# Kernel optimization log

Hardware: AMD Instinct MI355X
Metric: run time of the kernel (lower is better)

The kernel has to match this reference:

```python
import jax, jax.numpy as jnp
import numpy as np
import math

OVERLAP_RATIO = 0.5
TAU_OVERLAP = 0.07
TAU_TILE = 0.2
TILE_LOSS_WEIGHT = 0.1


def setup_inputs() -> dict:
    key = jax.random.key(0)
    k1, k2 = jax.random.split(key)
    B, V, S, D = 8, 8, 576, 768
    z1 = jax.random.normal(k1, (B * V, S, D), dtype=jnp.float32)
    z2 = jax.random.normal(k2, (B * V, S, D), dtype=jnp.float32)
    # module expects L2-normalised projections
    z1 = z1 / jnp.linalg.norm(z1, axis=-1, keepdims=True)
    z2 = z2 / jnp.linalg.norm(z2, axis=-1, keepdims=True)
    return {"z1": z1, "z2": z2, "batch_size": B, "num_views": V}


def _sym_infonce_diag(logits):
    # logits: [..., N, N]; labels are the diagonal (same index positives).
    lse_q = jax.nn.logsumexp(logits, axis=-1)  # row-wise (q -> k)
    lse_k = jax.nn.logsumexp(logits, axis=-2)  # col-wise (k -> q), no transpose copy
    diag = jnp.diagonal(logits, axis1=-2, axis2=-1)
    return 0.5 * (jnp.mean(lse_q - diag) + jnp.mean(lse_k - diag))


def reference(z1, z2, batch_size, num_views):
    B, V = batch_size, num_views
    z1 = z1.astype(jnp.float32)
    z2 = z2.astype(jnp.float32)
    BV, S, D = z1.shape
    H = W = int(math.isqrt(S))

    # ---- overlap InfoNCE (circular adjacency) ----
    g1 = z1.reshape(B, V, H, W, D)
    g2 = z2.reshape(B, V, H, W, D)
    k = max(1, int(W * OVERLAP_RATIO))
    N = B * H * k
    curr_right = g1[:, :, :, -k:, :]                      # [B,V,H,k,D]
    next_left = jnp.roll(g2, -1, axis=1)[:, :, :, :k, :]  # [B,V,H,k,D]
    Q = jnp.transpose(curr_right, (1, 0, 2, 3, 4)).reshape(V, N, D)
    K = jnp.transpose(next_left, (1, 0, 2, 3, 4)).reshape(V, N, D)
    ov_logits = jnp.einsum('vnd,vmd->vnm', Q, K) / TAU_OVERLAP  # [V,N,N]
    L_overlap = _sym_infonce_diag(ov_logits)

    # ---- within-tile InfoNCE ----
    tile_logits = jnp.einsum('bsd,btd->bst', z1, z2) / TAU_TILE  # [BV,S,S]
    L_tile = _sym_infonce_diag(tile_logits)

    total = L_overlap + TILE_LOSS_WEIGHT * L_tile
    return total
```

## Files before the change

### kernel.cpp

```cpp
#include <hip/hip_runtime.h>
#include <hip/hip_bf16.h>

typedef __attribute__((ext_vector_type(8))) short bf16x8_t;
typedef __attribute__((ext_vector_type(4))) float f32x4_t;
typedef __attribute__((ext_vector_type(8))) unsigned short u16x8_t;

__device__ inline unsigned short bfr(float f) {
    __hip_bfloat16 h = __float2bfloat16(f);
    return *reinterpret_cast<unsigned short*>(&h);
}

__device__ inline u16x8_t cvt8(float4 x, float4 y) {
    u16x8_t v;
    v[0] = bfr(x.x); v[1] = bfr(x.y); v[2] = bfr(x.z); v[3] = bfr(x.w);
    v[4] = bfr(y.x); v[5] = bfr(y.y); v[6] = bfr(y.z); v[7] = bfr(y.w);
    return v;
}

__global__ __launch_bounds__(256, 4) void gemm128_lse_all(
    const float* __restrict__ z1, const float* __restrict__ z2,
    float* __restrict__ ws) {
    const int tid  = threadIdx.x;
    const int lane = tid & 63;
    const int w    = tid >> 6;
    const int wM   = w >> 1;
    const int wN   = w & 1;
    const int lr   = lane & 15;
    const int lg   = lane >> 4;

    const int bid = blockIdx.x;
    const int lb  = (bid & 7) * 524 + (bid >> 3);

    int M, batch, brow, bcol;
    float inv_tau;
    float *rs, *cs, *dg;
    bool ov = (lb < 2592);
    if (ov) {
        M = 2304; inv_tau = 1.0f / 0.07f;
        rs = ws; cs = ws + 18432; dg = ws + 36864;
        batch = lb / 324;
        int rem = lb - batch * 324;
        int sc = rem / 108, r2 = rem - sc * 108;
        brow = r2 / 6;
        bcol = sc * 6 + (r2 - brow * 6);
    } else {
        M = 576; inv_tau = 1.0f / 0.2f;
        rs = ws + 55296; cs = ws + 92160; dg = ws + 129024;
        int tl = lb - 2592;
        batch = tl / 25;
        int rem = tl - batch * 25;
        brow = rem / 5;
        bcol = rem - brow * 5;
    }

    __shared__ unsigned short smem[16384];
    __shared__ int offA[128], offB[128];

    if (tid < 128) {
        int r = brow * 128 + tid;
        int off;
        if (ov) {
            int b = r / 288, rm = r % 288, h = rm / 12, j = rm % 12;
            off = ((b * 8 + batch) * 576 + h * 24 + 12 + j) * 768;
        } else {
            off = ((r < M) ? (batch * 576 + r) : (batch * 576)) * 768;
        }
        offA[tid] = off;
    } else {
        int c = bcol * 128 + (tid - 128);
        int off;
        if (ov) {
            int b = c / 288, rm = c % 288, h = rm / 12, j = rm % 12;
            off = ((b * 8 + ((batch + 1) & 7)) * 576 + h * 24 + j) * 768;
        } else {
            off = ((c < M) ? (batch * 576 + c) : (batch * 576)) * 768;
        }
        offB[tid - 128] = off;
    }
    __syncthreads();

    const int lrow8 = lane >> 3;
    const int cswz  = (((lane & 7) ^ lrow8) << 3);
    int sA[4], sB[4], dA[4], dB[4];
#pragma unroll
    for (int ra = 0; ra < 4; ++ra) {
        sA[ra] = offA[w * 32 + ra * 8 + lrow8] + cswz;
        sB[ra] = offB[w * 32 + ra * 8 + lrow8] + cswz;
        dA[ra] = (w * 32 + ra * 8) * 64 + lane * 8;
        dB[ra] = 8192 + (w * 32 + ra * 8) * 64 + lane * 8;
    }

    int aoff[2][4], boff[2][4];
#pragma unroll
    for (int h = 0; h < 2; ++h) {
#pragma unroll
        for (int i = 0; i < 4; ++i) {
            int ra = wM * 64 + i * 16 + lr;
            aoff[h][i] = ra * 64 + (((h * 4 + lg) ^ (ra & 7)) << 3);
            int rb = wN * 64 + i * 16 + lr;
            boff[h][i] = 8192 + rb * 64 + (((h * 4 + lg) ^ (rb & 7)) << 3);
        }
    }

    f32x4_t acc[4][4];
#pragma unroll
    for (int i = 0; i < 4; ++i)
#pragma unroll
        for (int j = 0; j < 4; ++j) acc[i][j] = (f32x4_t){0.f, 0.f, 0.f, 0.f};

    for (int t = 0; t < 12; ++t) {
        const int k0 = t * 64;
        {
            float4 fa[8];
#pragma unroll
            for (int ra = 0; ra < 4; ++ra) {
                fa[2 * ra]     = *(const float4*)(z1 + sA[ra] + k0);
                fa[2 * ra + 1] = *(const float4*)(z1 + sA[ra] + k0 + 4);
            }
#pragma unroll
            for (int ra = 0; ra < 4; ++ra)
                *(u16x8_t*)&smem[dA[ra]] = cvt8(fa[2 * ra], fa[2 * ra + 1]);
        }
        {
            float4 fb[8];
#pragma unroll
            for (int ra = 0; ra < 4; ++ra) {
                fb[2 * ra]     = *(const float4*)(z2 + sB[ra] + k0);
                fb[2 * ra + 1] = *(const float4*)(z2 + sB[ra] + k0 + 4);
            }
#pragma unroll
            for (int ra = 0; ra < 4; ++ra)
                *(u16x8_t*)&smem[dB[ra]] = cvt8(fb[2 * ra], fb[2 * ra + 1]);
        }
        __syncthreads();
#pragma unroll
        for (int h = 0; h < 2; ++h) {
            bf16x8_t av[4], bv[4];
#pragma unroll
            for (int i = 0; i < 4; ++i) av[i] = *(const bf16x8_t*)&smem[aoff[h][i]];
#pragma unroll
            for (int j = 0; j < 4; ++j) bv[j] = *(const bf16x8_t*)&smem[boff[h][j]];
            __builtin_amdgcn_s_setprio(1);
#pragma unroll
            for (int i = 0; i < 4; ++i)
#pragma unroll
                for (int j = 0; j < 4; ++j)
                    acc[i][j] = __builtin_amdgcn_mfma_f32_16x16x32_bf16(
                        av[i], bv[j], acc[i][j], 0, 0, 0);
            __builtin_amdgcn_s_setprio(0);
        }
        __syncthreads();
    }

    const int rowbase = brow * 128 + wM * 64;
    const int colbase = bcol * 128 + wN * 64;
    float colacc[4] = {0.f, 0.f, 0.f, 0.f};
#pragma unroll
    for (int i = 0; i < 4; ++i) {
#pragma unroll
        for (int reg = 0; reg < 4; ++reg) {
            int row = rowbase + i * 16 + lg * 4 + reg;
            bool rv = row < M;
            float rp = 0.f;
#pragma unroll
            for (int j = 0; j < 4; ++j) {
                int col = colbase + j * 16 + lr;
                float L = acc[i][j][reg] * inv_tau;
                float e = (rv && (col < M)) ? __expf(L) : 0.f;
                rp += e;
                colacc[j] += e;
                if (rv && row == col) dg[batch * M + row] = L;
            }
#pragma unroll
            for (int s = 1; s < 16; s <<= 1) rp += __shfl_xor(rp, s);
            if (lr == 0 && rv) atomicAdd(&rs[batch * M + row], rp);
        }
    }
#pragma unroll
    for (int j = 0; j < 4; ++j) {
        float cv = colacc[j];
        cv += __shfl_xor(cv, 16);
        cv += __shfl_xor(cv, 32);
        int col = colbase + j * 16 + lr;
        if (lg == 0 && col < M) atomicAdd(&cs[batch * M + col], cv);
    }
}

__global__ __launch_bounds__(256) void finalize_kernel(
    const float* __restrict__ ws, float* __restrict__ out) {
    const float* rs_ov = ws;
    const float* cs_ov = ws + 18432;
    const float* dg_ov = ws + 36864;
    const float* rs_t  = ws + 55296;
    const float* cs_t  = ws + 92160;
    const float* dg_t  = ws + 129024;
    const int g0 = blockIdx.x * blockDim.x + threadIdx.x;
    const int gs = gridDim.x * blockDim.x;
    float s_ov = 0.f, s_t = 0.f;
    for (int i = g0; i < 18432; i += gs)
        s_ov += logf(rs_ov[i]) + logf(cs_ov[i]) - 2.f * dg_ov[i];
    for (int i = g0; i < 36864; i += gs)
        s_t += logf(rs_t[i]) + logf(cs_t[i]) - 2.f * dg_t[i];
    float c = 0.5f * s_ov / 18432.f + 0.05f * s_t / 36864.f;
#pragma unroll
    for (int s = 1; s < 64; s <<= 1) c += __shfl_xor(c, s);
    __shared__ float red[4];
    int wv = threadIdx.x >> 6;
    if ((threadIdx.x & 63) == 0) red[wv] = c;
    __syncthreads();
    if (threadIdx.x == 0)
        atomicAdd(out, red[0] + red[1] + red[2] + red[3]);
}

extern "C" void kernel_launch(void* const* d_in, const int* in_sizes, int n_in,
                              void* d_out, int out_size, void* d_ws, size_t ws_size,
                              hipStream_t stream) {
    const float* z1 = (const float*)d_in[0];
    const float* z2 = (const float*)d_in[1];
    float* out = (float*)d_out;
    float* ws  = (float*)d_ws;

    const size_t ACC_B = 165888 * sizeof(float);
    hipMemsetAsync(d_ws, 0, ACC_B, stream);
    hipMemsetAsync(d_out, 0, sizeof(float), stream);

    gemm128_lse_all<<<4192, 256, 0, stream>>>(z1, z2, ws);
    finalize_kernel<<<16, 256, 0, stream>>>(ws, out);
}
```

Baseline: 189.1 us.

## Enlarge GEMM tile to 256x256 with 1024-thread blocks and double-buffered LDS

Each block now computes a 256x256 output tile with 16 waves instead of 128x128 with 4 waves, so each global fp32 element is loaded and converted to bf16 about half as often. The K loop uses 32-wide slices with two LDS buffers, staging the next slice before computing the current one, which removes one barrier per step. The cost is a much lower block count (1224 vs 4192), one block per CU, more padding waste on the 576-wide tile GEMMs (3x3 tiles of 256 cover 768), and more barrier steps over the shorter K slices.

```diff
diff --git a/kernel.cpp b/kernel.cpp
--- a/kernel.cpp
+++ b/kernel.cpp
@@ -17,47 +17,47 @@
     return v;
 }
 
-__global__ __launch_bounds__(256, 4) void gemm128_lse_all(
+__global__ __launch_bounds__(1024, 1) void gemm256_lse_all(
     const float* __restrict__ z1, const float* __restrict__ z2,
     float* __restrict__ ws) {
     const int tid  = threadIdx.x;
     const int lane = tid & 63;
     const int w    = tid >> 6;
-    const int wM   = w >> 1;
-    const int wN   = w & 1;
+    const int wr   = w >> 2;
+    const int wc   = w & 3;
     const int lr   = lane & 15;
     const int lg   = lane >> 4;
 
     const int bid = blockIdx.x;
-    const int lb  = (bid & 7) * 524 + (bid >> 3);
+    const int lb  = (bid & 7) * 153 + (bid >> 3);
 
     int M, batch, brow, bcol;
     float inv_tau;
     float *rs, *cs, *dg;
-    bool ov = (lb < 2592);
+    bool ov = (lb < 648);
     if (ov) {
         M = 2304; inv_tau = 1.0f / 0.07f;
         rs = ws; cs = ws + 18432; dg = ws + 36864;
-        batch = lb / 324;
-        int rem = lb - batch * 324;
-        int sc = rem / 108, r2 = rem - sc * 108;
-        brow = r2 / 6;
-        bcol = sc * 6 + (r2 - brow * 6);
+        batch = lb / 81;
+        int rem = lb - batch * 81;
+        int sc = rem / 27, r2 = rem - sc * 27;
+        brow = r2 / 3;
+        bcol = sc * 3 + (r2 - brow * 3);
     } else {
         M = 576; inv_tau = 1.0f / 0.2f;
         rs = ws + 55296; cs = ws + 92160; dg = ws + 129024;
-        int tl = lb - 2592;
-        batch = tl / 25;
-        int rem = tl - batch * 25;
-        brow = rem / 5;
-        bcol = rem - brow * 5;
-    }
-
-    __shared__ unsigned short smem[16384];
-    __shared__ int offA[128], offB[128];
-
-    if (tid < 128) {
-        int r = brow * 128 + tid;
+        int tl = lb - 648;
+        batch = tl / 9;
+        int rem = tl - batch * 9;
+        brow = rem / 3;
+        bcol = rem - brow * 3;
+    }
+
+    __shared__ unsigned short smem[32768];
+    __shared__ int offA[256], offB[256];
+
+    if (tid < 256) {
+        int r = brow * 256 + tid;
         int off;
         if (ov) {
             int b = r / 288, rm = r % 288, h = rm / 12, j = rm % 12;
@@ -66,8 +66,8 @@
             off = ((r < M) ? (batch * 576 + r) : (batch * 576)) * 768;
         }
         offA[tid] = off;
-    } else {
-        int c = bcol * 128 + (tid - 128);
+    } else if (tid < 512) {
+        int c = bcol * 256 + (tid - 256);
         int off;
         if (ov) {
             int b = c / 288, rm = c % 288, h = rm / 12, j = rm % 12;
@@ -75,31 +75,24 @@
         } else {
             off = ((c < M) ? (batch * 576 + c) : (batch * 576)) * 768;
         }
-        offB[tid - 128] = off;
+        offB[tid - 256] = off;
     }
     __syncthreads();
 
-    const int lrow8 = lane >> 3;
-    const int cswz  = (((lane & 7) ^ lrow8) << 3);
-    int sA[4], sB[4], dA[4], dB[4];
-#pragma unroll
-    for (int ra = 0; ra < 4; ++ra) {
-        sA[ra] = offA[w * 32 + ra * 8 + lrow8] + cswz;
-        sB[ra] = offB[w * 32 + ra * 8 + lrow8] + cswz;
-        dA[ra] = (w * 32 + ra * 8) * 64 + lane * 8;
-        dB[ra] = 8192 + (w * 32 + ra * 8) * 64 + lane * 8;
-    }
-
-    int aoff[2][4], boff[2][4];
-#pragma unroll
-    for (int h = 0; h < 2; ++h) {
-#pragma unroll
-        for (int i = 0; i < 4; ++i) {
-            int ra = wM * 64 + i * 16 + lr;
-            aoff[h][i] = ra * 64 + (((h * 4 + lg) ^ (ra & 7)) << 3);
-            int rb = wN * 64 + i * 16 + lr;
-            boff[h][i] = 8192 + rb * 64 + (((h * 4 + lg) ^ (rb & 7)) << 3);
-        }
+    const int srow = tid >> 2;
+    const int sc4  = ((tid & 3) ^ ((srow >> 1) & 3)) << 3;
+    const int srcA = offA[srow] + sc4;
+    const int srcB = offB[srow] + sc4;
+    const int dstA = srow * 32 + (tid & 3) * 8;
+    const int dstB = 8192 + dstA;
+
+    int aoff[4], boff[4];
+#pragma unroll
+    for (int i = 0; i < 4; ++i) {
+        int ra = wr * 64 + i * 16 + lr;
+        aoff[i] = ra * 32 + ((lg ^ ((ra >> 1) & 3)) << 3);
+        int rb = wc * 64 + i * 16 + lr;
+        boff[i] = 8192 + rb * 32 + ((lg ^ ((rb >> 1) & 3)) << 3);
     }
 
     f32x4_t acc[4][4];
@@ -108,52 +101,41 @@
 #pragma unroll
         for (int j = 0; j < 4; ++j) acc[i][j] = (f32x4_t){0.f, 0.f, 0.f, 0.f};
 
-    for (int t = 0; t < 12; ++t) {
-        const int k0 = t * 64;
-        {
-            float4 fa[8];
-#pragma unroll
-            for (int ra = 0; ra < 4; ++ra) {
-                fa[2 * ra]     = *(const float4*)(z1 + sA[ra] + k0);
-                fa[2 * ra + 1] = *(const float4*)(z1 + sA[ra] + k0 + 4);
-            }
-#pragma unroll
-            for (int ra = 0; ra < 4; ++ra)
-                *(u16x8_t*)&smem[dA[ra]] = cvt8(fa[2 * ra], fa[2 * ra + 1]);
-        }
-        {
-            float4 fb[8];
-#pragma unroll
-            for (int ra = 0; ra < 4; ++ra) {
-                fb[2 * ra]     = *(const float4*)(z2 + sB[ra] + k0);
-                fb[2 * ra + 1] = *(const float4*)(z2 + sB[ra] + k0 + 4);
-            }
-#pragma unroll
-            for (int ra = 0; ra < 4; ++ra)
-                *(u16x8_t*)&smem[dB[ra]] = cvt8(fb[2 * ra], fb[2 * ra + 1]);
-        }
+#define STG(T) do { \
+    const int sl_ = ((T) & 1) << 14; const int k0_ = (T) * 32; \
+    float4 fa0 = *(const float4*)(z1 + srcA + k0_); \
+    float4 fa1 = *(const float4*)(z1 + srcA + k0_ + 4); \
+    float4 fb0 = *(const float4*)(z2 + srcB + k0_); \
+    float4 fb1 = *(const float4*)(z2 + srcB + k0_ + 4); \
+    *(u16x8_t*)&smem[sl_ + dstA] = cvt8(fa0, fa1); \
+    *(u16x8_t*)&smem[sl_ + dstB] = cvt8(fb0, fb1); \
+} while (0)
+
+    STG(0);
+    __syncthreads();
+
+    for (int t = 0; t < 24; ++t) {
+        const unsigned short* S = &smem[(t & 1) << 14];
+        if (t < 23) STG(t + 1);
+        bf16x8_t av[4], bv[4];
+#pragma unroll
+        for (int i = 0; i < 4; ++i) av[i] = *(const bf16x8_t*)&S[aoff[i]];
+#pragma unroll
+        for (int j = 0; j < 4; ++j) bv[j] = *(const bf16x8_t*)&S[boff[j]];
+        __builtin_amdgcn_s_setprio(1);
+#pragma unroll
+        for (int i = 0; i < 4; ++i)
+#pragma unroll
+            for (int j = 0; j < 4; ++j)
+                acc[i][j] = __builtin_amdgcn_mfma_f32_16x16x32_bf16(
+                    av[i], bv[j], acc[i][j], 0, 0, 0);
+        __builtin_amdgcn_s_setprio(0);
         __syncthreads();
-#pragma unroll
-        for (int h = 0; h < 2; ++h) {
-            bf16x8_t av[4], bv[4];
-#pragma unroll
-            for (int i = 0; i < 4; ++i) av[i] = *(const bf16x8_t*)&smem[aoff[h][i]];
-#pragma unroll
-            for (int j = 0; j < 4; ++j) bv[j] = *(const bf16x8_t*)&smem[boff[h][j]];
-            __builtin_amdgcn_s_setprio(1);
-#pragma unroll
-            for (int i = 0; i < 4; ++i)
-#pragma unroll
-                for (int j = 0; j < 4; ++j)
-                    acc[i][j] = __builtin_amdgcn_mfma_f32_16x16x32_bf16(
-                        av[i], bv[j], acc[i][j], 0, 0, 0);
-            __builtin_amdgcn_s_setprio(0);
-        }
-        __syncthreads();
-    }
-
-    const int rowbase = brow * 128 + wM * 64;
-    const int colbase = bcol * 128 + wN * 64;
+    }
+#undef STG
+
+    const int rowbase = brow * 256 + wr * 64;
+    const int colbase = bcol * 256 + wc * 64;
     float colacc[4] = {0.f, 0.f, 0.f, 0.f};
 #pragma unroll
     for (int i = 0; i < 4; ++i) {
@@ -224,6 +206,6 @@
     hipMemsetAsync(d_ws, 0, ACC_B, stream);
     hipMemsetAsync(d_out, 0, sizeof(float), stream);
 
-    gemm128_lse_all<<<4192, 256, 0, stream>>>(z1, z2, ws);
+    gemm256_lse_all<<<1224, 1024, 0, stream>>>(z1, z2, ws);
     finalize_kernel<<<16, 256, 0, stream>>>(ws, out);
 }
```

New measurement: 203.5 us. 1.08x slower.
